# Performance work log

Hardware: AMD Instinct MI355X
Metric: run time of the kernel (lower is better)

## Reference

```python
import jax, jax.numpy as jnp
import numpy as np

EPS = 1e-5

def layernorm(x, g, b):
    mu = jnp.mean(x, axis=-1, keepdims=True)
    var = jnp.mean(jnp.square(x - mu), axis=-1, keepdims=True)
    return (x - mu) * jax.lax.rsqrt(var + EPS) * g + b

def rope(x):
    # x: [B, H, S, hd]; faithful to source: theta = 10000**(-2*pos/hd), pos in {0,2,4,...}
    S, hd = x.shape[-2], x.shape[-1]
    pos2 = jnp.arange(0, hd, 2, dtype=jnp.float32)
    theta = jnp.power(10000.0, -2.0 * pos2 / hd)          # [hd/2]
    ang = jnp.arange(S, dtype=jnp.float32)[:, None] * theta  # [S, hd/2]
    cos, sin = jnp.cos(ang), jnp.sin(ang)                  # broadcast over B,H
    xr = x.reshape(*x.shape[:-1], hd // 2, 2)
    x0, x1 = xr[..., 0], xr[..., 1]
    out = jnp.stack([x0 * cos - x1 * sin, x1 * cos + x0 * sin], axis=-1)
    return out.reshape(x.shape)

def setup_inputs() -> dict:
    key = jax.random.key(0)
    ks = jax.random.split(key, 8)
    B, S, D, H = 2, 2048, 1024, 16
    hd = D // H
    s_in = 1.0 / np.sqrt(D)
    s_h = 1.0 / np.sqrt(2 * D)
    return {
        "x": jax.random.normal(ks[0], (B, S, D), jnp.float32),
        "ln1_g": jnp.ones((D,), jnp.float32),
        "ln1_b": jnp.zeros((D,), jnp.float32),
        "Wq": jax.random.normal(ks[1], (H, D, hd), jnp.float32) * s_in,
        "Wk": jax.random.normal(ks[2], (H, D, hd), jnp.float32) * s_in,
        "Wv": jax.random.normal(ks[3], (H, D, hd), jnp.float32) * s_in,
        "Wo": jax.random.normal(ks[4], (D, D), jnp.float32) * s_in,
        "ln2_g": jnp.ones((D,), jnp.float32),
        "ln2_b": jnp.zeros((D,), jnp.float32),
        "W1": jax.random.normal(ks[5], (D, 2 * D), jnp.float32) * s_in,
        "W2": jax.random.normal(ks[6], (D, 2 * D), jnp.float32) * s_in,
        "W3": jax.random.normal(ks[7], (2 * D, D), jnp.float32) * s_h,
    }

def reference(x, ln1_g, ln1_b, Wq, Wk, Wv, Wo, ln2_g, ln2_b, W1, W2, W3):
    B, S, D = x.shape
    # --- attention sublayer ---
    h = layernorm(x, ln1_g, ln1_b)
    q = jnp.einsum("bsd,hdk->bhsk", h, Wq)
    k = jnp.einsum("bsd,hdk->bhsk", h, Wk)
    v = jnp.einsum("bsd,hdk->bhsk", h, Wv)
    q, k = rope(q), rope(k)
    hd = q.shape[-1]
    scores = jnp.einsum("bhqk,bhsk->bhqs", q, k) * (hd ** -0.5)  # [B,H,S,S]
    causal = jnp.tril(jnp.ones((S, S), bool))
    scores = jnp.where(causal, scores, jnp.float32(-jnp.inf))
    attn = jax.nn.softmax(scores, axis=-1)
    o = jnp.einsum("bhqs,bhsk->bhqk", attn, v)                   # [B,H,S,hd]
    o = o.transpose(0, 2, 1, 3).reshape(B, S, D)                 # concat heads
    x = x + o @ Wo
    # --- SwiGLU FFN sublayer ---
    h2 = layernorm(x, ln2_g, ln2_b)
    u = h2 @ W1
    ffn = (u * jax.nn.sigmoid(u)) * (h2 @ W2)
    return x + ffn @ W3
```

## Files before the change

### kernel.cpp

```cpp
#include <hip/hip_runtime.h>
#include <hip/hip_bf16.h>

using bf16 = __hip_bfloat16;
typedef __attribute__((ext_vector_type(8))) short bf16x8;
typedef __attribute__((ext_vector_type(4))) float f32x4;


__device__ inline float toF(float x) { return x; }
__device__ inline float toF(bf16 x) { return __bfloat162float(x); }

__device__ __forceinline__ void unpack8(uint4 u, float* f) {
    f[0] = __uint_as_float(u.x << 16); f[1] = __uint_as_float(u.x & 0xffff0000u);
    f[2] = __uint_as_float(u.y << 16); f[3] = __uint_as_float(u.y & 0xffff0000u);
    f[4] = __uint_as_float(u.z << 16); f[5] = __uint_as_float(u.z & 0xffff0000u);
    f[6] = __uint_as_float(u.w << 16); f[7] = __uint_as_float(u.w & 0xffff0000u);
}

__device__ __forceinline__ uint4 packbf8(const float* f) {
    union { unsigned short u[8]; uint4 v; } r;
#pragma unroll
    for (int i = 0; i < 8; i++) {
        bf16 b = __float2bfloat16(f[i]);
        r.u[i] = *(unsigned short*)&b;
    }
    return r.v;
}

__device__ __forceinline__ unsigned pack2(float lo, float hi) {
    bf16 a = __float2bfloat16(lo), b = __float2bfloat16(hi);
    return ((unsigned)*(unsigned short*)&b << 16) | (unsigned)*(unsigned short*)&a;
}

__device__ __forceinline__ void gl_lds16(const void* g, void* l) {
    __builtin_amdgcn_global_load_lds(
        (__attribute__((address_space(1))) void*)g,
        (__attribute__((address_space(3))) void*)l, 16, 0, 0);
}

template <typename Tx>
__device__ __forceinline__ void ln_body(
    const Tx* __restrict__ x, const float* __restrict__ g,
    const float* __restrict__ b, bf16* __restrict__ out, int row,
    float* s1, float* s2)
{
    const int D = 1024;
    int tid = threadIdx.x;
    const Tx* xr = x + (size_t)row * D;

    float vals[4];
    float sum = 0.f, sumsq = 0.f;
#pragma unroll
    for (int i = 0; i < 4; i++) {
        float v = toF(xr[tid + i * 256]);
        vals[i] = v; sum += v; sumsq += v * v;
    }
#pragma unroll
    for (int off = 32; off > 0; off >>= 1) {
        sum += __shfl_xor(sum, off);
        sumsq += __shfl_xor(sumsq, off);
    }
    int wave = tid >> 6, lane = tid & 63;
    if (lane == 0) { s1[wave] = sum; s2[wave] = sumsq; }
    __syncthreads();
    sum = s1[0] + s1[1] + s1[2] + s1[3];
    sumsq = s2[0] + s2[1] + s2[2] + s2[3];

    float mu = sum * (1.f / D);
    float var = sumsq * (1.f / D) - mu * mu;
    float rstd = rsqrtf(var + 1e-5f);

    bf16* orow = out + (size_t)row * D;
#pragma unroll
    for (int i = 0; i < 4; i++) {
        int c = tid + i * 256;
        orow[c] = __float2bfloat16((vals[i] - mu) * rstd * g[c] + b[c]);
    }
}

__global__ __launch_bounds__(256) void prep1_kernel(
    const float* __restrict__ x, const float* __restrict__ g,
    const float* __restrict__ b, bf16* __restrict__ h0, bf16* __restrict__ h1,
    const float* __restrict__ Wq, const float* __restrict__ Wk,
    const float* __restrict__ Wv, bf16* __restrict__ wt)
{
    __shared__ float t[32][33];
    __shared__ float s1[4], s2[4];
    int bx = blockIdx.x;
    if (bx < 4096) {
        int bb = bx >> 11, row = bx & 2047;
        ln_body<float>(x + ((size_t)bb << 21), g, b, bb ? h1 : h0, row, s1, s2);
        return;
    }
    int zz = bx - 4096;
    int z = zz >> 6, rem = zz & 63;
    int yy = rem >> 1, xx = rem & 1;
    const float* s = (z < 16) ? Wq : (z < 32) ? Wk : Wv;
    const float* ip = s + (size_t)(z & 15) * 65536;
    bf16* op = wt + ((size_t)z << 16);
    int c0 = xx * 32, r0 = yy * 32;
    int tx = threadIdx.x & 31, ty = threadIdx.x >> 5;
#pragma unroll
    for (int i = 0; i < 4; i++)
        t[ty + 8 * i][tx] = ip[(size_t)(r0 + ty + 8 * i) * 64 + c0 + tx];
    __syncthreads();
#pragma unroll
    for (int i = 0; i < 4; i++)
        op[(size_t)(c0 + ty + 8 * i) * 1024 + r0 + tx] = __float2bfloat16(t[tx][ty + 8 * i]);
}

__global__ __launch_bounds__(256) void prep2_kernel(
    const bf16* __restrict__ x2, const float* __restrict__ g,
    const float* __restrict__ b, bf16* __restrict__ h2,
    const float* __restrict__ W1, const float* __restrict__ W2,
    bf16* __restrict__ wt)
{
    __shared__ float t[32][33];
    __shared__ float s1[4], s2[4];
    int bx = blockIdx.x;
    if (bx < 2048) {
        ln_body<bf16>(x2, g, b, h2, bx, s1, s2);
        return;
    }
    int zz = bx - 2048;
    int xx = zz & 63, yy = (zz >> 6) & 31, z = zz >> 11;
    const float* ip = z ? W2 : W1;
    bf16* op = wt + ((size_t)z << 21);
    int c0 = xx * 32, r0 = yy * 32;
    int tx = threadIdx.x & 31, ty = threadIdx.x >> 5;
#pragma unroll
    for (int i = 0; i < 4; i++)
        t[ty + 8 * i][tx] = ip[(size_t)(r0 + ty + 8 * i) * 2048 + c0 + tx];
    __syncthreads();
#pragma unroll
    for (int i = 0; i < 4; i++)
        op[(size_t)(c0 + ty + 8 * i) * 1024 + r0 + tx] = __float2bfloat16(t[tx][ty + 8 * i]);
}

__global__ __launch_bounds__(256) void tconv_kernel(
    const float* __restrict__ in, bf16* __restrict__ out, int R, int C)
{
    __shared__ float t[32][33];
    int c0 = blockIdx.x * 32, r0 = blockIdx.y * 32;
    int tx = threadIdx.x & 31, ty = threadIdx.x >> 5;
#pragma unroll
    for (int i = 0; i < 4; i++)
        t[ty + 8 * i][tx] = in[(size_t)(r0 + ty + 8 * i) * C + c0 + tx];
    __syncthreads();
#pragma unroll
    for (int i = 0; i < 4; i++)
        out[(size_t)(c0 + ty + 8 * i) * R + r0 + tx] = __float2bfloat16(t[tx][ty + 8 * i]);
}

__global__ __launch_bounds__(256) void tconv_wo_kernel(
    const float* __restrict__ Wo, bf16* __restrict__ out)
{
    __shared__ float t[32][33];
    int z = blockIdx.z;
    const float* ip = Wo + (size_t)z * 64;
    bf16* op = out + ((size_t)z << 16);
    int c0 = blockIdx.x * 32, r0 = blockIdx.y * 32;
    int tx = threadIdx.x & 31, ty = threadIdx.x >> 5;
#pragma unroll
    for (int i = 0; i < 4; i++)
        t[ty + 8 * i][tx] = ip[(size_t)(r0 + ty + 8 * i) * 1024 + c0 + tx];
    __syncthreads();
#pragma unroll
    for (int i = 0; i < 4; i++)
        op[(size_t)(c0 + ty + 8 * i) * 1024 + r0 + tx] = __float2bfloat16(t[tx][ty + 8 * i]);
}

template <int MODE>
__global__ __launch_bounds__(256) void mfma_gemm(
    const bf16* __restrict__ A, const bf16* __restrict__ BT0,
    void* __restrict__ Cv, const void* __restrict__ resv,
    const void* __restrict__ p5, void* __restrict__ p6,
    int M, int N, int K)
{
    constexpr int NB = (MODE == 5) ? 3 : 2;
    __shared__ bf16 smem[2][NB][64 * 64];
    int tid = threadIdx.x, lane = tid & 63, w = tid >> 6;
    int wm = w >> 1, wn = w & 1;
    int m0 = blockIdx.y * 64, n0 = blockIdx.x * 64;

    const bf16* Ap = A;
    const bf16* BT = BT0;
    bf16* Cq = nullptr;
    const float* resF = (const float*)resv;
    void* Cdst = Cv;
    if (MODE == 1) {
        int z = blockIdx.z;
        if (z >> 1) Ap = (const bf16*)resv;
        BT = BT0 + ((size_t)(z & 1) << 20);
        Cq = (bf16*)((z >> 1) ? p6 : Cv) + ((size_t)(z & 1) << 21);
    }
    if (MODE == 6) Cq = (bf16*)Cv;
    if (MODE == 2) {
        int z = blockIdx.z;
        if (z) { Ap = (const bf16*)p5; Cdst = p6; }
        resF = (const float*)resv + ((size_t)z << 21);
    }

    int lrow = lane >> 3;
    int lcb  = (lane & 7) ^ lrow;
    const bf16* Ag  = Ap + (size_t)(m0 + w * 8 + lrow) * K + lcb * 8;
    const bf16* Bg0 = BT + (size_t)(n0 + w * 8 + lrow) * K + lcb * 8;
    const bf16* B2g = (MODE == 5)
        ? (const bf16*)resv + (size_t)(n0 + w * 8 + lrow) * K + lcb * 8
        : nullptr;
    unsigned sbase = (unsigned)__builtin_amdgcn_readfirstlane(w * 8 * 128);
    char* smc = (char*)smem;

    f32x4 acc[2][2], acc2[2][2];
#pragma unroll
    for (int i = 0; i < 2; i++)
#pragma unroll
        for (int j = 0; j < 2; j++) {
            acc[i][j] = (f32x4){0.f, 0.f, 0.f, 0.f};
            if (MODE == 5) acc2[i][j] = (f32x4){0.f, 0.f, 0.f, 0.f};
        }

    int cidx = lane & 15, quad = lane >> 4;

    auto STAGE = [&](int buf, int k0) {
        char* p = smc + (size_t)buf * (NB * 8192) + sbase;
        gl_lds16(Ag + k0,                   p);
        gl_lds16(Ag + (size_t)32 * K + k0,  p + 4096);
        gl_lds16(Bg0 + k0,                  p + 8192);
        gl_lds16(Bg0 + (size_t)32 * K + k0, p + 12288);
        if (MODE == 5) {
            gl_lds16(B2g + k0,                  p + 16384);
            gl_lds16(B2g + (size_t)32 * K + k0, p + 20480);
        }
    };

    STAGE(0, 0);
    __syncthreads();
    int cur = 0;
    for (int k0 = 0; k0 < K; k0 += 64) {
        if (k0 + 64 < K) STAGE(cur ^ 1, k0 + 64);
        const bf16* Ab = (const bf16*)(smc + (size_t)cur * (NB * 8192));
        const bf16* Bb = Ab + 4096;
        const bf16* B2b = Ab + 8192;
#pragma unroll
        for (int kk = 0; kk < 2; kk++) {
            int pb = (kk * 4 + quad) ^ (cidx & 7);
            bf16x8 af[2], bfr[2], b2f[2];
#pragma unroll
            for (int i = 0; i < 2; i++)
                af[i] = *(const bf16x8*)&Ab[(wm * 32 + i * 16 + cidx) * 64 + pb * 8];
#pragma unroll
            for (int j = 0; j < 2; j++)
                bfr[j] = *(const bf16x8*)&Bb[(wn * 32 + j * 16 + cidx) * 64 + pb * 8];
            if (MODE == 5) {
#pragma unroll
                for (int j = 0; j < 2; j++)
                    b2f[j] = *(const bf16x8*)&B2b[(wn * 32 + j * 16 + cidx) * 64 + pb * 8];
            }
            __builtin_amdgcn_s_setprio(1);
#pragma unroll
            for (int i = 0; i < 2; i++)
#pragma unroll
                for (int j = 0; j < 2; j++) {
                    acc[i][j] = __builtin_amdgcn_mfma_f32_16x16x32_bf16(af[i], bfr[j], acc[i][j], 0, 0, 0);
                    if (MODE == 5)
                        acc2[i][j] = __builtin_amdgcn_mfma_f32_16x16x32_bf16(af[i], b2f[j], acc2[i][j], 0, 0, 0);
                }
            __builtin_amdgcn_s_setprio(0);
        }
        __syncthreads();
        cur ^= 1;
    }

    int rbase = quad * 4;
#pragma unroll
    for (int i = 0; i < 2; i++) {
#pragma unroll
        for (int j = 0; j < 2; j++) {
            int row0 = m0 + wm * 32 + i * 16 + rbase;
            int col = n0 + wn * 32 + j * 16 + cidx;
            if (MODE == 6) {
                int h_ = col >> 6, d = col & 63;
                uint2 t;
                t.x = pack2(acc[i][j][0], acc[i][j][1]);
                t.y = pack2(acc[i][j][2], acc[i][j][3]);
                *(uint2*)&Cq[(size_t)h_ * 131072 + (size_t)d * 2048 + row0] = t;
                continue;
            }
#pragma unroll
            for (int r = 0; r < 4; r++) {
                int row = row0 + r;
                float v = acc[i][j][r];
                size_t idx = (size_t)row * N + col;
                if (MODE == 1) {
                    int h_ = col >> 6, kk = col & 63;
                    float other = __shfl_xor(v, 1);
                    float p = (float)(kk >> 1);
                    float theta = __expf(p * -0.5756462732485114f);
                    float ang = (float)row * theta;
                    float c, sn; __sincosf(ang, &sn, &c);
                    float outv = (kk & 1) ? (v * c + other * sn) : (v * c - other * sn);
                    Cq[((size_t)h_ * 2048 + row) * 64 + kk] = __float2bfloat16(outv);
                } else if (MODE == 2) {
                    v += resF[idx];
                    ((bf16*)Cdst)[idx] = __float2bfloat16(v);
                } else if (MODE == 5) {
                    float g2 = acc2[i][j][r];
                    float sg = 1.f / (1.f + __expf(-v));
                    ((bf16*)Cv)[idx] = __float2bfloat16(v * sg * g2);
                } else {
                    v += __bfloat162float(((const bf16*)resv)[idx]);
                    ((float*)Cv)[idx] = v;
                }
            }
        }
    }
}

__global__ __launch_bounds__(256) void attn_kernel(
    const bf16* __restrict__ q0, const bf16* __restrict__ k0,
    const bf16* __restrict__ vt0, bf16* __restrict__ o0,
    const bf16* __restrict__ q1, const bf16* __restrict__ k1,
    const bf16* __restrict__ vt1, bf16* __restrict__ o1)
{
    const int S = 2048;
    __shared__ bf16 Ks[64 * 64];
    __shared__ bf16 Vs[64 * 64];
    __shared__ __align__(16) char QPbuf[64 * 72 * 2];

    int zb = blockIdx.z;
    const bf16* q = zb ? q1 : q0;
    const bf16* k = zb ? k1 : k0;
    const bf16* vt = zb ? vt1 : vt0;
    bf16* o = zb ? o1 : o0;

    int h = blockIdx.y;
    int qt = (h & 8) ? (int)blockIdx.x : 31 - (int)blockIdx.x;
    int tid = threadIdx.x, lane = tid & 63, w = tid >> 6;
    int quad = lane >> 4, cidx = lane & 15;
    int m0 = qt * 64;

    const bf16* qb = q + ((size_t)h * S + m0) * 64;
    const bf16* kb = k + (size_t)h * S * 64;
    const bf16* vtb = vt + (size_t)h * 64 * S;

    int srow = tid >> 2;
    int sg = (tid & 3) * 16;

    bf16 (*Qs)[72] = (bf16 (*)[72])QPbuf;
    {
        const uint4* src = (const uint4*)(qb + (size_t)srow * 64 + sg);
        uint4 u0 = src[0], u1 = src[1];
        float f[16]; unpack8(u0, f); unpack8(u1, f + 8);
#pragma unroll
        for (int i = 0; i < 16; i++) f[i] *= 0.125f * 1.44269504f;
        *(uint4*)&Qs[srow][sg] = packbf8(f);
        *(uint4*)&Qs[srow][sg + 8] = packbf8(f + 8);
    }
    bf16x8 bQ0 = *(const bf16x8*)&Qs[w * 16 + cidx][quad * 8];
    bf16x8 bQ1 = *(const bf16x8*)&Qs[w * 16 + cidx][32 + quad * 8];

    unsigned* Pst = (unsigned*)QPbuf + w * 576;

    int cb0 = (tid & 3) * 2;
    int sw0 = ((cb0)     ^ (srow & 7)) * 8;
    int sw1 = ((cb0 + 1) ^ (srow & 7)) * 8;
    int pb0 = ((quad)     ^ (cidx & 7)) * 8;
    int pb1 = ((4 + quad) ^ (cidx & 7)) * 8;

    float m_i = -INFINITY, l_i = 0.f;
    f32x4 Oc[4];
#pragma unroll
    for (int i = 0; i < 4; i++) Oc[i] = (f32x4){0.f, 0.f, 0.f, 0.f};

    uint4 ka0, ka1, va0, va1;
    {
        const uint4* ksrc = (const uint4*)(kb + (size_t)srow * 64 + sg);
        ka0 = ksrc[0]; ka1 = ksrc[1];
        const uint4* vsrc = (const uint4*)(vtb + (size_t)srow * S + sg);
        va0 = vsrc[0]; va1 = vsrc[1];
    }

    for (int kt = 0; kt <= qt; kt++) {
        __syncthreads();
        *(uint4*)&Ks[srow * 64 + sw0] = ka0;
        *(uint4*)&Ks[srow * 64 + sw1] = ka1;
        *(uint4*)&Vs[srow * 64 + sw0] = va0;
        *(uint4*)&Vs[srow * 64 + sw1] = va1;
        __syncthreads();
        if (kt < qt) {
            const uint4* kn = (const uint4*)(kb + (size_t)((kt + 1) * 64 + srow) * 64 + sg);
            ka0 = kn[0]; ka1 = kn[1];
            const uint4* vn = (const uint4*)(vtb + (size_t)srow * S + (kt + 1) * 64 + sg);
            va0 = vn[0]; va1 = vn[1];
        }

        f32x4 sc[4];
#pragma unroll
        for (int i = 0; i < 4; i++) {
            bf16x8 aK0 = *(const bf16x8*)&Ks[(i * 16 + cidx) * 64 + pb0];
            bf16x8 aK1 = *(const bf16x8*)&Ks[(i * 16 + cidx) * 64 + pb1];
            f32x4 z = (f32x4){0.f, 0.f, 0.f, 0.f};
            __builtin_amdgcn_s_setprio(1);
            z = __builtin_amdgcn_mfma_f32_16x16x32_bf16(aK0, bQ0, z, 0, 0, 0);
            z = __builtin_amdgcn_mfma_f32_16x16x32_bf16(aK1, bQ1, z, 0, 0, 0);
            __builtin_amdgcn_s_setprio(0);
            sc[i] = z;
        }

        if (kt == qt) {
#pragma unroll
            for (int i = 0; i < 4; i++)
#pragma unroll
                for (int r = 0; r < 4; r++)
                    if (i * 16 + quad * 4 + r > w * 16 + cidx) sc[i][r] = -INFINITY;
        }

        float l0 = fmaxf(fmaxf(sc[0][0], sc[0][1]), fmaxf(sc[0][2], sc[0][3]));
        float l1 = fmaxf(fmaxf(sc[1][0], sc[1][1]), fmaxf(sc[1][2], sc[1][3]));
        float l2 = fmaxf(fmaxf(sc[2][0], sc[2][1]), fmaxf(sc[2][2], sc[2][3]));
        float l3 = fmaxf(fmaxf(sc[3][0], sc[3][1]), fmaxf(sc[3][2], sc[3][3]));
        float lmax = fmaxf(fmaxf(l0, l1), fmaxf(l2, l3));

        if (!__all(lmax <= m_i + 8.f)) {
            float pmax = fmaxf(lmax, __shfl_xor(lmax, 16));
            pmax = fmaxf(pmax, __shfl_xor(pmax, 32));
            float mnew = fmaxf(m_i, pmax);
            float alpha = __builtin_amdgcn_exp2f(m_i - mnew);
            l_i *= alpha;
#pragma unroll
            for (int i = 0; i < 4; i++) {
                Oc[i][0] *= alpha; Oc[i][1] *= alpha;
                Oc[i][2] *= alpha; Oc[i][3] *= alpha;
            }
            m_i = mnew;
        }

        float rs = 0.f;
#pragma unroll
        for (int i = 0; i < 4; i++)
#pragma unroll
            for (int r = 0; r < 4; r++) {
                sc[i][r] = __builtin_amdgcn_exp2f(sc[i][r] - m_i);
                rs += sc[i][r];
            }
        l_i += rs;

#pragma unroll
        for (int i = 0; i < 4; i++) {
            uint2 t;
            t.x = pack2(sc[i][0], sc[i][1]);
            t.y = pack2(sc[i][2], sc[i][3]);
            *(uint2*)&Pst[cidx * 36 + 8 * i + 2 * quad] = t;
        }
        bf16x8 bP0 = *(const bf16x8*)&Pst[cidx * 36 + 4 * quad];
        bf16x8 bP1 = *(const bf16x8*)&Pst[cidx * 36 + 16 + 4 * quad];

#pragma unroll
        for (int i = 0; i < 4; i++) {
            bf16x8 aV0 = *(const bf16x8*)&Vs[(i * 16 + cidx) * 64 + pb0];
            bf16x8 aV1 = *(const bf16x8*)&Vs[(i * 16 + cidx) * 64 + pb1];
            __builtin_amdgcn_s_setprio(1);
            Oc[i] = __builtin_amdgcn_mfma_f32_16x16x32_bf16(aV0, bP0, Oc[i], 0, 0, 0);
            Oc[i] = __builtin_amdgcn_mfma_f32_16x16x32_bf16(aV1, bP1, Oc[i], 0, 0, 0);
            __builtin_amdgcn_s_setprio(0);
        }
    }

    float lr = l_i;
    lr += __shfl_xor(lr, 16);
    lr += __shfl_xor(lr, 32);
    float inv = 1.f / lr;
#pragma unroll
    for (int i = 0; i < 4; i++) {
        uint2 t;
        t.x = pack2(Oc[i][0] * inv, Oc[i][1] * inv);
        t.y = pack2(Oc[i][2] * inv, Oc[i][3] * inv);
        *(uint2*)&Pst[cidx * 36 + 8 * i + 2 * quad] = t;
    }
    int r2 = lane >> 2, g2 = (lane & 3) * 8;
    uint4 o0v = *(const uint4*)&Pst[r2 * 36 + g2];
    uint4 o1v = *(const uint4*)&Pst[r2 * 36 + g2 + 4];
    bf16* orow = o + (size_t)(m0 + w * 16 + r2) * 1024 + h * 64;
    *(uint4*)(orow + g2 * 2) = o0v;
    *(uint4*)(orow + g2 * 2 + 8) = o1v;
}

extern "C" void kernel_launch(void* const* d_in, const int* in_sizes, int n_in,
                              void* d_out, int out_size, void* d_ws, size_t ws_size,
                              hipStream_t stream)
{
    const int S = 2048;

    const float* x    = (const float*)d_in[0];
    const float* ln1g = (const float*)d_in[1];
    const float* ln1b = (const float*)d_in[2];
    const float* Wq   = (const float*)d_in[3];
    const float* Wk   = (const float*)d_in[4];
    const float* Wv   = (const float*)d_in[5];
    const float* Wo   = (const float*)d_in[6];
    const float* ln2g = (const float*)d_in[7];
    const float* ln2b = (const float*)d_in[8];
    const float* W1   = (const float*)d_in[9];
    const float* W2   = (const float*)d_in[10];
    const float* W3   = (const float*)d_in[11];
    float* out = (float*)d_out;

    const size_t M2 = 1u << 21;
    bf16* r0 = (bf16*)d_ws;
    bf16* r1 = r0 + M2;
    bf16* r2 = r1 + M2;
    bf16* r3 = r2 + M2;
    bf16* pb0 = (bf16*)out;
    bf16* pb1 = pb0 + 2 * M2;
    float* out0 = out;
    float* out1 = out + (1u << 21);

    prep1_kernel<<<7168, 256, 0, stream>>>(x, ln1g, ln1b, r0, r1,
                                           Wq, Wk, Wv, pb0);

    mfma_gemm<1><<<dim3(16, 32, 4), 256, 0, stream>>>(
        r0, pb0, r2, r1, nullptr, pb1, S, 1024, 1024);

    mfma_gemm<6><<<dim3(16, 32, 1), 256, 0, stream>>>(
        r0, pb0 + M2, pb0, nullptr, nullptr, nullptr, S, 1024, 1024);

    mfma_gemm<6><<<dim3(16, 32, 1), 256, 0, stream>>>(
        r1, pb0 + M2, r0, nullptr, nullptr, nullptr, S, 1024, 1024);

    attn_kernel<<<dim3(32, 16, 2), 256, 0, stream>>>(
        r2, r3, pb0, r1, pb1, pb1 + M2, r0, pb0 + M2);

    tconv_wo_kernel<<<dim3(2, 32, 16), 256, 0, stream>>>(Wo, r2);

    mfma_gemm<2><<<dim3(16, 32, 2), 256, 0, stream>>>(
        r1, r2, r3, x, pb0 + M2, r0, S, 1024, 1024);

    prep2_kernel<<<6144, 256, 0, stream>>>(r3, ln2g, ln2b, pb1, W1, W2, pb0);

    mfma_gemm<5><<<dim3(32, 32, 1), 256, 0, stream>>>(
        pb1, pb0, r1, pb0 + M2, nullptr, nullptr, S, 2048, 1024);

    tconv_kernel<<<dim3(32, 64), 256, 0, stream>>>(W3, pb1 + M2, 2048, 1024);

    mfma_gemm<4><<<dim3(16, 32, 1), 256, 0, stream>>>(
        r1, pb1 + M2, out0, r3, nullptr, nullptr, S, 1024, 2048);

    prep2_kernel<<<6144, 256, 0, stream>>>(r0, ln2g, ln2b, r3, W1, W2, pb1);

    mfma_gemm<5><<<dim3(32, 32, 1), 256, 0, stream>>>(
        r3, pb1, r1, pb1 + M2, nullptr, nullptr, S, 2048, 1024);

    tconv_kernel<<<dim3(32, 64), 256, 0, stream>>>(W3, r3, 2048, 1024);

    mfma_gemm<4><<<dim3(16, 32, 1), 256, 0, stream>>>(
        r1, r3, out1, r0, nullptr, nullptr, S, 1024, 2048);
}
```

Measured before the change: 327.0 us.

## Process 128 query rows per attention block and fuse W3 transpose into prep2

```diff
diff --git a/kernel.cpp b/kernel.cpp
--- a/kernel.cpp
+++ b/kernel.cpp
@@ -112,7 +112,8 @@
     const bf16* __restrict__ x2, const float* __restrict__ g,
     const float* __restrict__ b, bf16* __restrict__ h2,
     const float* __restrict__ W1, const float* __restrict__ W2,
-    bf16* __restrict__ wt)
+    bf16* __restrict__ wt, const float* __restrict__ W3,
+    bf16* __restrict__ w3t)
 {
     __shared__ float t[32][33];
     __shared__ float s1[4], s2[4];
@@ -121,19 +122,32 @@
         ln_body<bf16>(x2, g, b, h2, bx, s1, s2);
         return;
     }
+    int tx = threadIdx.x & 31, ty = threadIdx.x >> 5;
     int zz = bx - 2048;
-    int xx = zz & 63, yy = (zz >> 6) & 31, z = zz >> 11;
-    const float* ip = z ? W2 : W1;
-    bf16* op = wt + ((size_t)z << 21);
+    if (zz < 4096) {
+        int xx = zz & 63, yy = (zz >> 6) & 31, z = zz >> 11;
+        const float* ip = z ? W2 : W1;
+        bf16* op = wt + ((size_t)z << 21);
+        int c0 = xx * 32, r0 = yy * 32;
+#pragma unroll
+        for (int i = 0; i < 4; i++)
+            t[ty + 8 * i][tx] = ip[(size_t)(r0 + ty + 8 * i) * 2048 + c0 + tx];
+        __syncthreads();
+#pragma unroll
+        for (int i = 0; i < 4; i++)
+            op[(size_t)(c0 + ty + 8 * i) * 1024 + r0 + tx] = __float2bfloat16(t[tx][ty + 8 * i]);
+        return;
+    }
+    int idx = zz - 4096;
+    int xx = idx & 31, yy = idx >> 5;
     int c0 = xx * 32, r0 = yy * 32;
-    int tx = threadIdx.x & 31, ty = threadIdx.x >> 5;
-#pragma unroll
-    for (int i = 0; i < 4; i++)
-        t[ty + 8 * i][tx] = ip[(size_t)(r0 + ty + 8 * i) * 2048 + c0 + tx];
+#pragma unroll
+    for (int i = 0; i < 4; i++)
+        t[ty + 8 * i][tx] = W3[(size_t)(r0 + ty + 8 * i) * 1024 + c0 + tx];
     __syncthreads();
 #pragma unroll
     for (int i = 0; i < 4; i++)
-        op[(size_t)(c0 + ty + 8 * i) * 1024 + r0 + tx] = __float2bfloat16(t[tx][ty + 8 * i]);
+        w3t[(size_t)(c0 + ty + 8 * i) * 2048 + r0 + tx] = __float2bfloat16(t[tx][ty + 8 * i]);
 }
 
 __global__ __launch_bounds__(256) void tconv_kernel(
@@ -316,7 +330,7 @@
     }
 }
 
-__global__ __launch_bounds__(256) void attn_kernel(
+__global__ __launch_bounds__(256, 2) void attn_kernel(
     const bf16* __restrict__ q0, const bf16* __restrict__ k0,
     const bf16* __restrict__ vt0, bf16* __restrict__ o0,
     const bf16* __restrict__ q1, const bf16* __restrict__ k1,
@@ -325,7 +339,7 @@
     const int S = 2048;
     __shared__ bf16 Ks[64 * 64];
     __shared__ bf16 Vs[64 * 64];
-    __shared__ __align__(16) char QPbuf[64 * 72 * 2];
+    __shared__ __align__(16) char QPbuf[128 * 72 * 2];
 
     int zb = blockIdx.z;
     const bf16* q = zb ? q1 : q0;
@@ -334,10 +348,10 @@
     bf16* o = zb ? o1 : o0;
 
     int h = blockIdx.y;
-    int qt = (h & 8) ? (int)blockIdx.x : 31 - (int)blockIdx.x;
+    int qt = zb ? (int)blockIdx.x : 15 - (int)blockIdx.x;
     int tid = threadIdx.x, lane = tid & 63, w = tid >> 6;
     int quad = lane >> 4, cidx = lane & 15;
-    int m0 = qt * 64;
+    int m0 = qt * 128;
 
     const bf16* qb = q + ((size_t)h * S + m0) * 64;
     const bf16* kb = k + (size_t)h * S * 64;
@@ -348,18 +362,26 @@
 
     bf16 (*Qs)[72] = (bf16 (*)[72])QPbuf;
     {
-        const uint4* src = (const uint4*)(qb + (size_t)srow * 64 + sg);
-        uint4 u0 = src[0], u1 = src[1];
-        float f[16]; unpack8(u0, f); unpack8(u1, f + 8);
-#pragma unroll
-        for (int i = 0; i < 16; i++) f[i] *= 0.125f * 1.44269504f;
-        *(uint4*)&Qs[srow][sg] = packbf8(f);
-        *(uint4*)&Qs[srow][sg + 8] = packbf8(f + 8);
-    }
-    bf16x8 bQ0 = *(const bf16x8*)&Qs[w * 16 + cidx][quad * 8];
-    bf16x8 bQ1 = *(const bf16x8*)&Qs[w * 16 + cidx][32 + quad * 8];
-
-    unsigned* Pst = (unsigned*)QPbuf + w * 576;
+        int srow2 = tid >> 1, sg2 = (tid & 1) * 32;
+        const uint4* src = (const uint4*)(qb + (size_t)srow2 * 64 + sg2);
+#pragma unroll
+        for (int p = 0; p < 2; p++) {
+            uint4 u0 = src[2 * p], u1 = src[2 * p + 1];
+            float f[16]; unpack8(u0, f); unpack8(u1, f + 8);
+#pragma unroll
+            for (int i = 0; i < 16; i++) f[i] *= 0.125f * 1.44269504f;
+            *(uint4*)&Qs[srow2][sg2 + 16 * p] = packbf8(f);
+            *(uint4*)&Qs[srow2][sg2 + 16 * p + 8] = packbf8(f + 8);
+        }
+    }
+    bf16x8 bQ[2][2];
+#pragma unroll
+    for (int hf = 0; hf < 2; hf++) {
+        bQ[hf][0] = *(const bf16x8*)&Qs[w * 32 + hf * 16 + cidx][quad * 8];
+        bQ[hf][1] = *(const bf16x8*)&Qs[w * 32 + hf * 16 + cidx][32 + quad * 8];
+    }
+
+    unsigned* Pst = (unsigned*)QPbuf + w * (32 * 36);
 
     int cb0 = (tid & 3) * 2;
     int sw0 = ((cb0)     ^ (srow & 7)) * 8;
@@ -367,10 +389,15 @@
     int pb0 = ((quad)     ^ (cidx & 7)) * 8;
     int pb1 = ((4 + quad) ^ (cidx & 7)) * 8;
 
-    float m_i = -INFINITY, l_i = 0.f;
-    f32x4 Oc[4];
-#pragma unroll
-    for (int i = 0; i < 4; i++) Oc[i] = (f32x4){0.f, 0.f, 0.f, 0.f};
+    float m_i[2] = {-INFINITY, -INFINITY};
+    float l_i[2] = {0.f, 0.f};
+    f32x4 Oc[2][4];
+#pragma unroll
+    for (int hf = 0; hf < 2; hf++)
+#pragma unroll
+        for (int i = 0; i < 4; i++) Oc[hf][i] = (f32x4){0.f, 0.f, 0.f, 0.f};
+
+    int nt = 2 * qt + 2;
 
     uint4 ka0, ka1, va0, va1;
     {
@@ -380,109 +407,131 @@
         va0 = vsrc[0]; va1 = vsrc[1];
     }
 
-    for (int kt = 0; kt <= qt; kt++) {
+    for (int kt = 0; kt < nt; kt++) {
         __syncthreads();
         *(uint4*)&Ks[srow * 64 + sw0] = ka0;
         *(uint4*)&Ks[srow * 64 + sw1] = ka1;
         *(uint4*)&Vs[srow * 64 + sw0] = va0;
         *(uint4*)&Vs[srow * 64 + sw1] = va1;
         __syncthreads();
-        if (kt < qt) {
+        if (kt + 1 < nt) {
             const uint4* kn = (const uint4*)(kb + (size_t)((kt + 1) * 64 + srow) * 64 + sg);
             ka0 = kn[0]; ka1 = kn[1];
             const uint4* vn = (const uint4*)(vtb + (size_t)srow * S + (kt + 1) * 64 + sg);
             va0 = vn[0]; va1 = vn[1];
         }
 
-        f32x4 sc[4];
+        f32x4 sc[2][4];
 #pragma unroll
         for (int i = 0; i < 4; i++) {
             bf16x8 aK0 = *(const bf16x8*)&Ks[(i * 16 + cidx) * 64 + pb0];
             bf16x8 aK1 = *(const bf16x8*)&Ks[(i * 16 + cidx) * 64 + pb1];
-            f32x4 z = (f32x4){0.f, 0.f, 0.f, 0.f};
             __builtin_amdgcn_s_setprio(1);
-            z = __builtin_amdgcn_mfma_f32_16x16x32_bf16(aK0, bQ0, z, 0, 0, 0);
-            z = __builtin_amdgcn_mfma_f32_16x16x32_bf16(aK1, bQ1, z, 0, 0, 0);
+#pragma unroll
+            for (int hf = 0; hf < 2; hf++) {
+                f32x4 z = (f32x4){0.f, 0.f, 0.f, 0.f};
+                z = __builtin_amdgcn_mfma_f32_16x16x32_bf16(aK0, bQ[hf][0], z, 0, 0, 0);
+                z = __builtin_amdgcn_mfma_f32_16x16x32_bf16(aK1, bQ[hf][1], z, 0, 0, 0);
+                sc[hf][i] = z;
+            }
             __builtin_amdgcn_s_setprio(0);
-            sc[i] = z;
-        }
-
-        if (kt == qt) {
+        }
+
+        if (kt >= nt - 2) {
+#pragma unroll
+            for (int hf = 0; hf < 2; hf++) {
+                int qpos = m0 + w * 32 + hf * 16 + cidx;
+#pragma unroll
+                for (int i = 0; i < 4; i++)
+#pragma unroll
+                    for (int r = 0; r < 4; r++)
+                        if (kt * 64 + i * 16 + quad * 4 + r > qpos)
+                            sc[hf][i][r] = -INFINITY;
+            }
+        }
+
+#pragma unroll
+        for (int hf = 0; hf < 2; hf++) {
+            float l0 = fmaxf(fmaxf(sc[hf][0][0], sc[hf][0][1]), fmaxf(sc[hf][0][2], sc[hf][0][3]));
+            float l1 = fmaxf(fmaxf(sc[hf][1][0], sc[hf][1][1]), fmaxf(sc[hf][1][2], sc[hf][1][3]));
+            float l2 = fmaxf(fmaxf(sc[hf][2][0], sc[hf][2][1]), fmaxf(sc[hf][2][2], sc[hf][2][3]));
+            float l3 = fmaxf(fmaxf(sc[hf][3][0], sc[hf][3][1]), fmaxf(sc[hf][3][2], sc[hf][3][3]));
+            float lmax = fmaxf(fmaxf(l0, l1), fmaxf(l2, l3));
+
+            if (!__all(lmax <= m_i[hf] + 8.f)) {
+                float pmax = fmaxf(lmax, __shfl_xor(lmax, 16));
+                pmax = fmaxf(pmax, __shfl_xor(pmax, 32));
+                float mnew = fmaxf(m_i[hf], pmax);
+                float alpha = __builtin_amdgcn_exp2f(m_i[hf] - mnew);
+                l_i[hf] *= alpha;
+#pragma unroll
+                for (int i = 0; i < 4; i++) {
+                    Oc[hf][i][0] *= alpha; Oc[hf][i][1] *= alpha;
+                    Oc[hf][i][2] *= alpha; Oc[hf][i][3] *= alpha;
+                }
+                m_i[hf] = mnew;
+            }
+
+            float rs = 0.f;
 #pragma unroll
             for (int i = 0; i < 4; i++)
 #pragma unroll
-                for (int r = 0; r < 4; r++)
-                    if (i * 16 + quad * 4 + r > w * 16 + cidx) sc[i][r] = -INFINITY;
-        }
-
-        float l0 = fmaxf(fmaxf(sc[0][0], sc[0][1]), fmaxf(sc[0][2], sc[0][3]));
-        float l1 = fmaxf(fmaxf(sc[1][0], sc[1][1]), fmaxf(sc[1][2], sc[1][3]));
-        float l2 = fmaxf(fmaxf(sc[2][0], sc[2][1]), fmaxf(sc[2][2], sc[2][3]));
-        float l3 = fmaxf(fmaxf(sc[3][0], sc[3][1]), fmaxf(sc[3][2], sc[3][3]));
-        float lmax = fmaxf(fmaxf(l0, l1), fmaxf(l2, l3));
-
-        if (!__all(lmax <= m_i + 8.f)) {
-            float pmax = fmaxf(lmax, __shfl_xor(lmax, 16));
-            pmax = fmaxf(pmax, __shfl_xor(pmax, 32));
-            float mnew = fmaxf(m_i, pmax);
-            float alpha = __builtin_amdgcn_exp2f(m_i - mnew);
-            l_i *= alpha;
+                for (int r = 0; r < 4; r++) {
+                    sc[hf][i][r] = __builtin_amdgcn_exp2f(sc[hf][i][r] - m_i[hf]);
+                    rs += sc[hf][i][r];
+                }
+            l_i[hf] += rs;
+
 #pragma unroll
             for (int i = 0; i < 4; i++) {
-                Oc[i][0] *= alpha; Oc[i][1] *= alpha;
-                Oc[i][2] *= alpha; Oc[i][3] *= alpha;
-            }
-            m_i = mnew;
-        }
-
-        float rs = 0.f;
-#pragma unroll
-        for (int i = 0; i < 4; i++)
-#pragma unroll
-            for (int r = 0; r < 4; r++) {
-                sc[i][r] = __builtin_amdgcn_exp2f(sc[i][r] - m_i);
-                rs += sc[i][r];
-            }
-        l_i += rs;
-
-#pragma unroll
-        for (int i = 0; i < 4; i++) {
-            uint2 t;
-            t.x = pack2(sc[i][0], sc[i][1]);
-            t.y = pack2(sc[i][2], sc[i][3]);
-            *(uint2*)&Pst[cidx * 36 + 8 * i + 2 * quad] = t;
-        }
-        bf16x8 bP0 = *(const bf16x8*)&Pst[cidx * 36 + 4 * quad];
-        bf16x8 bP1 = *(const bf16x8*)&Pst[cidx * 36 + 16 + 4 * quad];
+                uint2 t;
+                t.x = pack2(sc[hf][i][0], sc[hf][i][1]);
+                t.y = pack2(sc[hf][i][2], sc[hf][i][3]);
+                *(uint2*)&Pst[(hf * 16 + cidx) * 36 + 8 * i + 2 * quad] = t;
+            }
+        }
+
+        bf16x8 bP[2][2];
+#pragma unroll
+        for (int hf = 0; hf < 2; hf++) {
+            bP[hf][0] = *(const bf16x8*)&Pst[(hf * 16 + cidx) * 36 + 4 * quad];
+            bP[hf][1] = *(const bf16x8*)&Pst[(hf * 16 + cidx) * 36 + 16 + 4 * quad];
+        }
 
 #pragma unroll
         for (int i = 0; i < 4; i++) {
             bf16x8 aV0 = *(const bf16x8*)&Vs[(i * 16 + cidx) * 64 + pb0];
             bf16x8 aV1 = *(const bf16x8*)&Vs[(i * 16 + cidx) * 64 + pb1];
             __builtin_amdgcn_s_setprio(1);
-            Oc[i] = __builtin_amdgcn_mfma_f32_16x16x32_bf16(aV0, bP0, Oc[i], 0, 0, 0);
-            Oc[i] = __builtin_amdgcn_mfma_f32_16x16x32_bf16(aV1, bP1, Oc[i], 0, 0, 0);
+#pragma unroll
+            for (int hf = 0; hf < 2; hf++) {
+                Oc[hf][i] = __builtin_amdgcn_mfma_f32_16x16x32_bf16(aV0, bP[hf][0], Oc[hf][i], 0, 0, 0);
+                Oc[hf][i] = __builtin_amdgcn_mfma_f32_16x16x32_bf16(aV1, bP[hf][1], Oc[hf][i], 0, 0, 0);
+            }
             __builtin_amdgcn_s_setprio(0);
         }
     }
 
-    float lr = l_i;
-    lr += __shfl_xor(lr, 16);
-    lr += __shfl_xor(lr, 32);
-    float inv = 1.f / lr;
-#pragma unroll
-    for (int i = 0; i < 4; i++) {
-        uint2 t;
-        t.x = pack2(Oc[i][0] * inv, Oc[i][1] * inv);
-        t.y = pack2(Oc[i][2] * inv, Oc[i][3] * inv);
-        *(uint2*)&Pst[cidx * 36 + 8 * i + 2 * quad] = t;
-    }
     int r2 = lane >> 2, g2 = (lane & 3) * 8;
-    uint4 o0v = *(const uint4*)&Pst[r2 * 36 + g2];
-    uint4 o1v = *(const uint4*)&Pst[r2 * 36 + g2 + 4];
-    bf16* orow = o + (size_t)(m0 + w * 16 + r2) * 1024 + h * 64;
-    *(uint4*)(orow + g2 * 2) = o0v;
-    *(uint4*)(orow + g2 * 2 + 8) = o1v;
+#pragma unroll
+    for (int hf = 0; hf < 2; hf++) {
+        float lr = l_i[hf];
+        lr += __shfl_xor(lr, 16);
+        lr += __shfl_xor(lr, 32);
+        float inv = 1.f / lr;
+#pragma unroll
+        for (int i = 0; i < 4; i++) {
+            uint2 t;
+            t.x = pack2(Oc[hf][i][0] * inv, Oc[hf][i][1] * inv);
+            t.y = pack2(Oc[hf][i][2] * inv, Oc[hf][i][3] * inv);
+            *(uint2*)&Pst[(hf * 16 + cidx) * 36 + 8 * i + 2 * quad] = t;
+        }
+        uint4 o0v = *(const uint4*)&Pst[(hf * 16 + r2) * 36 + g2];
+        uint4 o1v = *(const uint4*)&Pst[(hf * 16 + r2) * 36 + g2 + 4];
+        bf16* orow = o + (size_t)(m0 + w * 32 + hf * 16 + r2) * 1024 + h * 64;
+        *(uint4*)(orow + g2 * 2) = o0v;
+        *(uint4*)(orow + g2 * 2 + 8) = o1v;
+    }
 }
 
 extern "C" void kernel_launch(void* const* d_in, const int* in_sizes, int n_in,
@@ -527,7 +576,7 @@
     mfma_gemm<6><<<dim3(16, 32, 1), 256, 0, stream>>>(
         r1, pb0 + M2, r0, nullptr, nullptr, nullptr, S, 1024, 1024);
 
-    attn_kernel<<<dim3(32, 16, 2), 256, 0, stream>>>(
+    attn_kernel<<<dim3(16, 16, 2), 256, 0, stream>>>(
         r2, r3, pb0, r1, pb1, pb1 + M2, r0, pb0 + M2);
 
     tconv_wo_kernel<<<dim3(2, 32, 16), 256, 0, stream>>>(Wo, r2);
@@ -535,17 +584,17 @@
     mfma_gemm<2><<<dim3(16, 32, 2), 256, 0, stream>>>(
         r1, r2, r3, x, pb0 + M2, r0, S, 1024, 1024);
 
-    prep2_kernel<<<6144, 256, 0, stream>>>(r3, ln2g, ln2b, pb1, W1, W2, pb0);
+    prep2_kernel<<<8192, 256, 0, stream>>>(r3, ln2g, ln2b, pb1, W1, W2, pb0,
+                                           W3, pb1 + M2);
 
     mfma_gemm<5><<<dim3(32, 32, 1), 256, 0, stream>>>(
         pb1, pb0, r1, pb0 + M2, nullptr, nullptr, S, 2048, 1024);
 
-    tconv_kernel<<<dim3(32, 64), 256, 0, stream>>>(W3, pb1 + M2, 2048, 1024);
-
     mfma_gemm<4><<<dim3(16, 32, 1), 256, 0, stream>>>(
         r1, pb1 + M2, out0, r3, nullptr, nullptr, S, 1024, 2048);
 
-    prep2_kernel<<<6144, 256, 0, stream>>>(r0, ln2g, ln2b, r3, W1, W2, pb1);
+    prep2_kernel<<<6144, 256, 0, stream>>>(r0, ln2g, ln2b, r3, W1, W2, pb1,
+                                           nullptr, nullptr);
 
     mfma_gemm<5><<<dim3(32, 32, 1), 256, 0, stream>>>(
         r3, pb1, r1, pb1 + M2, nullptr, nullptr, S, 2048, 1024);
```

Result: slower. 335.9 us (+2.7%).
